# Kernel tuning notes

Hardware: AMD Instinct MI355X
Metric: run time of the kernel (lower is better)

The kernel has to match this reference:

```python
import jax, jax.numpy as jnp
import numpy as np

TAU = 1.0      # temperature for gumbel-softmax
EPS = 1e-12    # F.normalize eps


def _l2norm(v, axis):
    n = jnp.sqrt(jnp.sum(v * v, axis=axis, keepdims=True))
    return v / jnp.maximum(n, EPS)


def setup_inputs() -> dict:
    key = jax.random.key(0)
    k1, k2, k3, k4 = jax.random.split(key, 4)
    b, c, h, w, n = 8, 512, 64, 64, 1024
    x = jax.random.normal(k1, (b, c, h, w), dtype=jnp.float32)
    centers = jax.random.normal(k2, (n, c), dtype=jnp.float32)          # VQ codebook
    clusters = jax.random.normal(k3, (n, c), dtype=jnp.float32)         # ClusterLookup param
    gumbel_noise = jax.random.gumbel(k4, (b, n, h, w), dtype=jnp.float32)
    return {"x": x, "centers": centers, "clusters": clusters, "gumbel_noise": gumbel_noise}


def reference(x, centers, clusters, gumbel_noise):
    # similarity logits: [b, n, h, w]
    inner = jnp.einsum('bchw,nc->bnhw', x, centers)
    # hard gumbel-softmax (straight-through) over code dim
    y_soft = jax.nn.softmax((inner + gumbel_noise) / TAU, axis=1)
    idx = jnp.argmax(y_soft, axis=1)                                     # [b, h, w]
    y_hard = jax.nn.one_hot(idx, centers.shape[0], axis=1, dtype=y_soft.dtype)
    one_hot = y_hard - jax.lax.stop_gradient(y_soft) + y_soft            # [b, n, h, w]
    # quantized features: codebook lookup expressed as einsum
    z_q = jnp.einsum('bnhw,nd->bdhw', one_hot, centers)                  # [b, c, h, w]
    # ClusterLookup(z_q, alpha=None, is_direct=False)
    nf = _l2norm(z_q, axis=1)
    ncl = _l2norm(clusters, axis=1)
    ip = jnp.einsum('bchw,nc->bnhw', nf, ncl)                            # cluster logits
    preds = jnp.argmax(ip, axis=1)                                       # [b, h, w] int
    probs = jax.nn.one_hot(preds, clusters.shape[0], axis=1, dtype=ip.dtype)
    cluster_loss = -jnp.mean(jnp.sum(probs * ip, axis=1))
    return (cluster_loss, preds, ip, z_q)
```

## Files before the change

### kernel.cpp

```cpp
#include <hip/hip_runtime.h>
#include <math.h>

#define C 512
#define HW 4096
#define N 1024
#define NPIX 32768
#define MARGIN 2.0f

typedef short s16x8 __attribute__((ext_vector_type(8)));
typedef float f32x4 __attribute__((ext_vector_type(4)));

__device__ inline unsigned short f2bf(float f) {
    unsigned int u = __float_as_uint(f);
    return (unsigned short)((u + 0x7FFFu + ((u >> 16) & 1u)) >> 16);
}
__device__ inline float h2f(unsigned short u) {
    _Float16 h; __builtin_memcpy(&h, &u, 2); return (float)h;
}
__device__ inline unsigned short f2h(float f) {
    _Float16 h = (_Float16)f; unsigned short u; __builtin_memcpy(&u, &h, 2); return u;
}
__device__ inline unsigned int mono(float v) {
    unsigned int u = __float_as_uint(v);
    return (u & 0x80000000u) ? ~u : (u | 0x80000000u);
}
__device__ inline void gload_lds16(const void* gsrc, void* ldst) {
    __builtin_amdgcn_global_load_lds(
        (const __attribute__((address_space(1))) unsigned int*)gsrc,
        (__attribute__((address_space(3))) unsigned int*)ldst, 16, 0, 0);
}

__global__ __launch_bounds__(64) void k_norms(const float* __restrict__ centers,
                                              const float* __restrict__ clusters,
                                              float* __restrict__ cnorm,
                                              float* __restrict__ clnorm) {
    int r = blockIdx.x;
    const float* src = (r < N) ? (centers + (size_t)r * C) : (clusters + (size_t)(r - N) * C);
    int lane = threadIdx.x;
    float s = 0.f;
    for (int k = lane; k < C; k += 64) { float v = src[k]; s += v * v; }
    #pragma unroll
    for (int m = 1; m < 64; m <<= 1) s += __shfl_xor(s, m, 64);
    if (lane == 0) {
        float nrm = sqrtf(s);
        if (nrm < 1e-12f) nrm = 1e-12f;
        if (r < N) cnorm[r] = nrm; else clnorm[r - N] = nrm;
    }
}

__global__ __launch_bounds__(256) void k_gemmM(const float* __restrict__ centers,
                                               const float* __restrict__ clusters,
                                               const float* __restrict__ cnorm,
                                               const float* __restrict__ clnorm,
                                               float* __restrict__ M) {
    __shared__ float as[32][68];
    __shared__ float bs[32][68];
    int tid = threadIdx.x;
    int tx = tid & 15, ty = tid >> 4;
    int i0 = blockIdx.x * 64, j0 = blockIdx.y * 64;
    int lrow = tid >> 2, lkq = (tid & 3) * 8;
    float acc[4][4] = {};
    for (int kc = 0; kc < C; kc += 32) {
        float4 a0 = *(const float4*)(centers + (size_t)(i0 + lrow) * C + kc + lkq);
        float4 a1 = *(const float4*)(centers + (size_t)(i0 + lrow) * C + kc + lkq + 4);
        float4 b0 = *(const float4*)(clusters + (size_t)(j0 + lrow) * C + kc + lkq);
        float4 b1 = *(const float4*)(clusters + (size_t)(j0 + lrow) * C + kc + lkq + 4);
        __syncthreads();
        as[lkq+0][lrow]=a0.x; as[lkq+1][lrow]=a0.y; as[lkq+2][lrow]=a0.z; as[lkq+3][lrow]=a0.w;
        as[lkq+4][lrow]=a1.x; as[lkq+5][lrow]=a1.y; as[lkq+6][lrow]=a1.z; as[lkq+7][lrow]=a1.w;
        bs[lkq+0][lrow]=b0.x; bs[lkq+1][lrow]=b0.y; bs[lkq+2][lrow]=b0.z; bs[lkq+3][lrow]=b0.w;
        bs[lkq+4][lrow]=b1.x; bs[lkq+5][lrow]=b1.y; bs[lkq+6][lrow]=b1.z; bs[lkq+7][lrow]=b1.w;
        __syncthreads();
        #pragma unroll
        for (int k = 0; k < 32; k += 4) {
            float av[4][4], bv[4][4];
            #pragma unroll
            for (int kk = 0; kk < 4; ++kk) {
                float4 ta = *(const float4*)&as[k+kk][tx*4];
                float4 tb = *(const float4*)&bs[k+kk][ty*4];
                av[kk][0]=ta.x; av[kk][1]=ta.y; av[kk][2]=ta.z; av[kk][3]=ta.w;
                bv[kk][0]=tb.x; bv[kk][1]=tb.y; bv[kk][2]=tb.z; bv[kk][3]=tb.w;
            }
            #pragma unroll
            for (int kk = 0; kk < 4; ++kk)
                #pragma unroll
                for (int ii = 0; ii < 4; ++ii)
                    #pragma unroll
                    for (int jj = 0; jj < 4; ++jj)
                        acc[ii][jj] = fmaf(av[kk][ii], bv[kk][jj], acc[ii][jj]);
        }
    }
    float rci[4], rcj[4];
    #pragma unroll
    for (int ii = 0; ii < 4; ++ii) rci[ii] = cnorm[i0 + tx*4 + ii];
    #pragma unroll
    for (int jj = 0; jj < 4; ++jj) rcj[jj] = clnorm[j0 + ty*4 + jj];
    #pragma unroll
    for (int ii = 0; ii < 4; ++ii)
        #pragma unroll
        for (int jj = 0; jj < 4; ++jj)
            M[(size_t)(i0 + tx*4 + ii) * N + (j0 + ty*4 + jj)] = acc[ii][jj] / (rci[ii] * rcj[jj]);
}

__global__ __launch_bounds__(256) void k_rowstat(const float* __restrict__ M,
                                                 float* __restrict__ rowmax,
                                                 int* __restrict__ rowarg) {
    __shared__ float sv[256];
    __shared__ int   sa[256];
    int i = blockIdx.x, tid = threadIdx.x;
    float bv = -INFINITY; int ba = 0;
    for (int j = tid; j < N; j += 256) {
        float v = M[(size_t)i * N + j];
        if (v > bv || (v == bv && j < ba)) { bv = v; ba = j; }
    }
    sv[tid] = bv; sa[tid] = ba;
    __syncthreads();
    for (int s = 128; s > 0; s >>= 1) {
        if (tid < s) {
            float v = sv[tid + s]; int a = sa[tid + s];
            if (v > sv[tid] || (v == sv[tid] && a < sa[tid])) { sv[tid] = v; sa[tid] = a; }
        }
        __syncthreads();
    }
    if (tid == 0) { rowmax[i] = sv[0]; rowarg[i] = sa[0]; }
}

__global__ __launch_bounds__(256) void k_prepT(const float* __restrict__ x,
                                               float* __restrict__ xT) {
    __shared__ float t[64][65];
    int bidx = blockIdx.x;
    int pt = bidx & 63, kt = (bidx >> 6) & 7, b = bidx >> 9;
    int r = threadIdx.x >> 4, c4 = (threadIdx.x & 15) * 4;
    const float* src = x + ((size_t)b * C + kt * 64) * HW + pt * 64;
    #pragma unroll
    for (int rr = 0; rr < 4; ++rr) {
        int row = rr * 16 + r;
        float4 v = *(const float4*)(src + (size_t)row * HW + c4);
        t[row][c4] = v.x; t[row][c4+1] = v.y; t[row][c4+2] = v.z; t[row][c4+3] = v.w;
    }
    __syncthreads();
    float* dst = xT + ((size_t)b * HW + pt * 64) * C + kt * 64;
    #pragma unroll
    for (int rr = 0; rr < 4; ++rr) {
        int row = rr * 16 + r;
        float4 v = { t[c4][row], t[c4+1][row], t[c4+2][row], t[c4+3][row] };
        *(float4*)(dst + (size_t)row * C + c4) = v;
    }
}

__global__ __launch_bounds__(64) void k_cenfrag(const float* __restrict__ centers,
                                                unsigned short* __restrict__ cenB) {
    int f = blockIdx.x;
    int nt = f >> 4, kt = f & 15;
    int lane = threadIdx.x;
    int r = lane & 15, g = lane >> 4;
    const float* src = centers + (size_t)(nt * 16 + r) * C + kt * 32 + g * 4;
    float4 lo = *(const float4*)src;
    float4 hi = *(const float4*)(src + 16);
    union { unsigned short us[8]; uint4 q; } u;
    u.us[0]=f2bf(lo.x); u.us[1]=f2bf(lo.y); u.us[2]=f2bf(lo.z); u.us[3]=f2bf(lo.w);
    u.us[4]=f2bf(hi.x); u.us[5]=f2bf(hi.y); u.us[6]=f2bf(hi.z); u.us[7]=f2bf(hi.w);
    *(uint4*)(cenB + ((size_t)f * 64 + lane) * 8) = u.q;
}

__global__ __launch_bounds__(256, 3) void k_fused(const float* __restrict__ xT,
                                                  const unsigned short* __restrict__ cenB,
                                                  const float* __restrict__ gumbel,
                                                  const float* __restrict__ centers,
                                                  int* __restrict__ idxb) {
    __shared__ unsigned short cen[2][8192];
    __shared__ float glds[2][1024];
    __shared__ unsigned long long pixkey[64];
    __shared__ unsigned int candlist[4][256];
    __shared__ int candcount[4];

    int tid = threadIdx.x;
    int lane = tid & 63, w = tid >> 6;
    int r = lane & 15, g = lane >> 4;

    int p0 = blockIdx.x * 64;
    int b = p0 >> 12, hw0 = p0 & (HW - 1);

    if (tid < 64) pixkey[tid] = 0ull;
    if (tid < 4) candcount[tid] = 0;

    int grow_ = tid >> 4;
    int gcol_ = ((tid ^ (tid >> 4)) & 15) * 4;
    const float* gbase = gumbel + (size_t)b * N * HW + hw0 + gcol_;

    {
        const char* src = (const char*)cenB + w * 4096 + lane * 16;
        char* dst = (char*)&cen[0][0] + w * 4096;
        #pragma unroll
        for (int i = 0; i < 4; ++i) gload_lds16(src + i * 1024, dst + i * 1024);
        gload_lds16(gbase + (size_t)grow_ * HW, (char*)&glds[0][0] + tid * 16);
    }

    s16x8 a[16];
    {
        const float* xrow = xT + (size_t)(p0 + w * 16 + r) * C;
        #pragma unroll
        for (int kt = 0; kt < 16; ++kt) {
            float4 lo = *(const float4*)(xrow + kt * 32 + g * 4);
            float4 hi = *(const float4*)(xrow + kt * 32 + 16 + g * 4);
            s16x8 t;
            t[0]=(short)f2bf(lo.x); t[1]=(short)f2bf(lo.y); t[2]=(short)f2bf(lo.z); t[3]=(short)f2bf(lo.w);
            t[4]=(short)f2bf(hi.x); t[5]=(short)f2bf(hi.y); t[6]=(short)f2bf(hi.z); t[7]=(short)f2bf(hi.w);
            a[kt] = t;
        }
    }
    __syncthreads();

    float m4[4] = {-INFINITY, -INFINITY, -INFINITY, -INFINITY};
    int cur = 0;
    int gswz = r * 64 + ((((w << 2) + g) ^ r) << 2);

    for (int tc = 0; tc < 8; ++tc) {
        unsigned int keepH[16];
        #pragma unroll
        for (int s = 0; s < 8; ++s) {
            int t = tc * 8 + s;
            if (t < 63) {
                const char* src = (const char*)cenB + (size_t)(t + 1) * 16384 + w * 4096 + lane * 16;
                char* dst = (char*)&cen[cur ^ 1][0] + w * 4096;
                #pragma unroll
                for (int i = 0; i < 4; ++i) gload_lds16(src + i * 1024, dst + i * 1024);
                gload_lds16(gbase + (size_t)((t + 1) * 16 + grow_) * HW,
                            (char*)&glds[cur ^ 1][0] + tid * 16);
            }
            const s16x8* bp = (const s16x8*)&cen[cur][0] + lane;
            f32x4 acc0 = {0.f,0.f,0.f,0.f}, acc1 = {0.f,0.f,0.f,0.f};
            #pragma unroll
            for (int kt = 0; kt < 16; kt += 2) {
                acc0 = __builtin_amdgcn_mfma_f32_16x16x32_bf16(a[kt],   bp[kt*64],     acc0, 0,0,0);
                acc1 = __builtin_amdgcn_mfma_f32_16x16x32_bf16(a[kt+1], bp[(kt+1)*64], acc1, 0,0,0);
            }
            f32x4 gv = *(const f32x4*)&glds[cur][gswz];
            float v0 = acc0[0]+acc1[0]+gv[0], v1 = acc0[1]+acc1[1]+gv[1];
            float v2 = acc0[2]+acc1[2]+gv[2], v3 = acc0[3]+acc1[3]+gv[3];
            m4[0]=fmaxf(m4[0],v0); m4[1]=fmaxf(m4[1],v1);
            m4[2]=fmaxf(m4[2],v2); m4[3]=fmaxf(m4[3],v3);
            keepH[s*2]   = (unsigned int)f2h(v0) | ((unsigned int)f2h(v1) << 16);
            keepH[s*2+1] = (unsigned int)f2h(v2) | ((unsigned int)f2h(v3) << 16);
            __syncthreads();
            cur ^= 1;
        }
        #pragma unroll
        for (int s2 = 1; s2 < 16; s2 <<= 1) {
            #pragma unroll
            for (int j = 0; j < 4; ++j) m4[j] = fmaxf(m4[j], __shfl_xor(m4[j], s2, 64));
        }
        float thr[4];
        #pragma unroll
        for (int j = 0; j < 4; ++j) thr[j] = m4[j] - MARGIN;
        #pragma unroll
        for (int s = 0; s < 8; ++s) {
            int nn = ((tc * 8 + s) << 4) + r;
            #pragma unroll
            for (int j2 = 0; j2 < 2; ++j2) {
                unsigned int pk = keepH[s * 2 + j2];
                float lo = h2f((unsigned short)(pk & 0xFFFFu));
                float hi = h2f((unsigned short)(pk >> 16));
                if (lo >= thr[j2 * 2]) {
                    int pos = atomicAdd(&candcount[w], 1);
                    if (pos < 256) candlist[w][pos] =
                        (unsigned int)nn | ((unsigned int)(w * 16 + g * 4 + j2 * 2) << 10);
                }
                if (hi >= thr[j2 * 2 + 1]) {
                    int pos = atomicAdd(&candcount[w], 1);
                    if (pos < 256) candlist[w][pos] =
                        (unsigned int)nn | ((unsigned int)(w * 16 + g * 4 + j2 * 2 + 1) << 10);
                }
            }
        }
    }

    int cc = candcount[w]; if (cc > 256) cc = 256;
    int sl = lane & 15, cg = lane >> 4;
    for (int t0 = 0; t0 < cc; t0 += 4) {
        int c = t0 + cg;
        bool valid = c < cc;
        unsigned int e = candlist[w][valid ? c : 0];
        int n = (int)(e & 1023u), pl = (int)(e >> 10);
        const float* xr = xT + (size_t)(p0 + pl) * C;
        const float* cenr = centers + (size_t)n * C;
        float s = 0.f;
        #pragma unroll
        for (int m = 0; m < 8; ++m) {
            int G = sl + (m << 4);
            float4 xv = *(const float4*)(xr + (G << 2));
            float4 cv = *(const float4*)(cenr + (G << 2));
            s = fmaf(xv.x, cv.x, s); s = fmaf(xv.y, cv.y, s);
            s = fmaf(xv.z, cv.z, s); s = fmaf(xv.w, cv.w, s);
        }
        #pragma unroll
        for (int s2 = 1; s2 < 16; s2 <<= 1) s += __shfl_xor(s, s2, 64);
        if (valid && sl == 0) {
            float val = s + gumbel[((size_t)b * N + n) * HW + hw0 + pl];
            unsigned long long key = ((unsigned long long)mono(val) << 32) | (unsigned int)(1023 - n);
            atomicMax(&pixkey[pl], key);
        }
    }
    __syncthreads();
    if (tid < 64) idxb[p0 + tid] = 1023 - (int)(unsigned int)(pixkey[tid] & 0xFFFFFFFFull);
}

__global__ __launch_bounds__(256) void k_preds(const int* __restrict__ idxb,
                                               const float* __restrict__ rowmax,
                                               const int* __restrict__ rowarg,
                                               float* __restrict__ preds_out,
                                               float* __restrict__ partial) {
    __shared__ float sv[256];
    int gid = blockIdx.x * 256 + threadIdx.x;
    int i = idxb[gid];
    preds_out[gid] = (float)rowarg[i];
    sv[threadIdx.x] = rowmax[i];
    __syncthreads();
    for (int s = 128; s > 0; s >>= 1) {
        if (threadIdx.x < s) sv[threadIdx.x] += sv[threadIdx.x + s];
        __syncthreads();
    }
    if (threadIdx.x == 0) partial[blockIdx.x] = sv[0];
}

__global__ __launch_bounds__(256) void k_gather(const float* __restrict__ src, int ncols,
                                                const int* __restrict__ idx,
                                                float* __restrict__ dst) {
    __shared__ float rows[64][65];
    int tile = blockIdx.x;
    int col0 = blockIdx.y * 64;
    int tid = threadIdx.x;
    int lane = tid & 63, w = tid >> 6;
    int b = tile >> 6, hw0 = (tile & 63) << 6;
    #pragma unroll
    for (int r8 = 0; r8 < 16; ++r8) {
        int r = w * 16 + r8;
        int row = idx[tile * 64 + r];
        rows[r][lane] = src[(size_t)row * ncols + col0 + lane];
    }
    __syncthreads();
    #pragma unroll
    for (int jj = 0; jj < 16; ++jj) {
        int j = col0 + w * 16 + jj;
        dst[((size_t)b * ncols + j) * HW + hw0 + lane] = rows[lane][w * 16 + jj];
    }
}

__global__ __launch_bounds__(128) void k_loss(const float* __restrict__ partial,
                                              float* __restrict__ out) {
    __shared__ float sv[128];
    sv[threadIdx.x] = partial[threadIdx.x];
    __syncthreads();
    for (int s = 64; s > 0; s >>= 1) {
        if (threadIdx.x < s) sv[threadIdx.x] += sv[threadIdx.x + s];
        __syncthreads();
    }
    if (threadIdx.x == 0) out[0] = -(sv[0] / 32768.0f);
}

extern "C" void kernel_launch(void* const* d_in, const int* in_sizes, int n_in,
                              void* d_out, int out_size, void* d_ws, size_t ws_size,
                              hipStream_t stream) {
    const float* x        = (const float*)d_in[0];
    const float* centers  = (const float*)d_in[1];
    const float* clusters = (const float*)d_in[2];
    const float* gumbel   = (const float*)d_in[3];
    float* out = (float*)d_out;

    char* w = (char*)d_ws;
    int*   idxb    = (int*)w;
    float* cnorm   = (float*)(w + 131072);
    float* clnorm  = cnorm + 1024;
    float* rowmax  = clnorm + 1024;
    int*   rowarg  = (int*)(rowmax + 1024);
    float* partial = (float*)(rowarg + 1024);
    float* M       = (float*)(w + 262144);
    unsigned short* cenB = (unsigned short*)(w + 4456448);

    float* out_loss  = out;
    float* out_preds = out + 1;
    float* out_ip    = out + 1 + 32768;
    float* out_zq    = out + 1 + 32768 + (size_t)N * NPIX;

    float* xT = out_zq;

    k_norms  <<<2048, 64, 0, stream>>>(centers, clusters, cnorm, clnorm);
    k_gemmM  <<<dim3(16, 16), 256, 0, stream>>>(centers, clusters, cnorm, clnorm, M);
    k_rowstat<<<1024, 256, 0, stream>>>(M, rowmax, rowarg);
    k_cenfrag<<<1024, 64, 0, stream>>>(centers, cenB);
    k_prepT  <<<4096, 256, 0, stream>>>(x, xT);
    k_fused  <<<512, 256, 0, stream>>>(xT, cenB, gumbel, centers, idxb);
    k_preds  <<<128, 256, 0, stream>>>(idxb, rowmax, rowarg, out_preds, partial);
    k_gather <<<dim3(512, 16), 256, 0, stream>>>(M, N, idxb, out_ip);
    k_gather <<<dim3(512, 8),  256, 0, stream>>>(centers, C, idxb, out_zq);
    k_loss   <<<1, 128, 0, stream>>>(partial, out_loss);
}
```

Measured before the change: 298.4 us.

## Triple-buffer codebook and gumbel tiles with two-stage-ahead async prefetch

Replaces the double-buffered LDS pipeline for codebook fragments and gumbel noise with a three-buffer ring that prefetches two tiles ahead. It uses explicit vmcnt/lgkmcnt waits and raw s_barrier instead of __syncthreads, and issues the initial prefetch after the x-fragment loads. The goal is to hide global-to-LDS latency behind the MFMA work. In exchange, LDS use rises and launch bounds drop from 3 to 2 blocks per CU, which lowers occupancy. The hand-written waitcnt counts must match the number of outstanding loads exactly.

```diff
diff --git a/kernel.cpp b/kernel.cpp
--- a/kernel.cpp
+++ b/kernel.cpp
@@ -163,13 +163,13 @@
     *(uint4*)(cenB + ((size_t)f * 64 + lane) * 8) = u.q;
 }
 
-__global__ __launch_bounds__(256, 3) void k_fused(const float* __restrict__ xT,
+__global__ __launch_bounds__(256, 2) void k_fused(const float* __restrict__ xT,
                                                   const unsigned short* __restrict__ cenB,
                                                   const float* __restrict__ gumbel,
                                                   const float* __restrict__ centers,
                                                   int* __restrict__ idxb) {
-    __shared__ unsigned short cen[2][8192];
-    __shared__ float glds[2][1024];
+    __shared__ unsigned short cen[3][8192];
+    __shared__ float glds[3][1024];
     __shared__ unsigned long long pixkey[64];
     __shared__ unsigned int candlist[4][256];
     __shared__ int candcount[4];
@@ -183,18 +183,6 @@
 
     if (tid < 64) pixkey[tid] = 0ull;
     if (tid < 4) candcount[tid] = 0;
-
-    int grow_ = tid >> 4;
-    int gcol_ = ((tid ^ (tid >> 4)) & 15) * 4;
-    const float* gbase = gumbel + (size_t)b * N * HW + hw0 + gcol_;
-
-    {
-        const char* src = (const char*)cenB + w * 4096 + lane * 16;
-        char* dst = (char*)&cen[0][0] + w * 4096;
-        #pragma unroll
-        for (int i = 0; i < 4; ++i) gload_lds16(src + i * 1024, dst + i * 1024);
-        gload_lds16(gbase + (size_t)grow_ * HW, (char*)&glds[0][0] + tid * 16);
-    }
 
     s16x8 a[16];
     {
@@ -209,10 +197,30 @@
             a[kt] = t;
         }
     }
-    __syncthreads();
+
+    int grow_ = tid >> 4;
+    int gcol_ = ((tid ^ (tid >> 4)) & 15) * 4;
+    const float* gbase = gumbel + (size_t)b * N * HW + hw0 + gcol_;
+
+    #define STAGE(T, BUF) { \
+        const char* s_ = (const char*)cenB + (size_t)(T) * 16384 + w * 4096 + lane * 16; \
+        char* d_ = (char*)&cen[0][0] + (BUF) * 16384 + w * 4096; \
+        gload_lds16(s_, d_); gload_lds16(s_ + 1024, d_ + 1024); \
+        gload_lds16(s_ + 2048, d_ + 2048); gload_lds16(s_ + 3072, d_ + 3072); \
+        gload_lds16(gbase + (size_t)((T) * 16 + grow_) * HW, \
+                    (char*)&glds[0][0] + (BUF) * 4096 + tid * 16); \
+    }
+
+    __builtin_amdgcn_sched_barrier(0);
+    STAGE(0, 0);
+    STAGE(1, 1);
+    __builtin_amdgcn_sched_barrier(0);
+    asm volatile("s_waitcnt vmcnt(5)" ::: "memory");
+    __builtin_amdgcn_s_barrier();
+    __builtin_amdgcn_sched_barrier(0);
 
     float m4[4] = {-INFINITY, -INFINITY, -INFINITY, -INFINITY};
-    int cur = 0;
+    int c0 = 0;
     int gswz = r * 64 + ((((w << 2) + g) ^ r) << 2);
 
     for (int tc = 0; tc < 8; ++tc) {
@@ -220,30 +228,32 @@
         #pragma unroll
         for (int s = 0; s < 8; ++s) {
             int t = tc * 8 + s;
-            if (t < 63) {
-                const char* src = (const char*)cenB + (size_t)(t + 1) * 16384 + w * 4096 + lane * 16;
-                char* dst = (char*)&cen[cur ^ 1][0] + w * 4096;
-                #pragma unroll
-                for (int i = 0; i < 4; ++i) gload_lds16(src + i * 1024, dst + i * 1024);
-                gload_lds16(gbase + (size_t)((t + 1) * 16 + grow_) * HW,
-                            (char*)&glds[cur ^ 1][0] + tid * 16);
-            }
-            const s16x8* bp = (const s16x8*)&cen[cur][0] + lane;
+            const s16x8* bp = (const s16x8*)((char*)&cen[0][0] + c0 * 16384) + lane;
             f32x4 acc0 = {0.f,0.f,0.f,0.f}, acc1 = {0.f,0.f,0.f,0.f};
             #pragma unroll
             for (int kt = 0; kt < 16; kt += 2) {
                 acc0 = __builtin_amdgcn_mfma_f32_16x16x32_bf16(a[kt],   bp[kt*64],     acc0, 0,0,0);
                 acc1 = __builtin_amdgcn_mfma_f32_16x16x32_bf16(a[kt+1], bp[(kt+1)*64], acc1, 0,0,0);
             }
-            f32x4 gv = *(const f32x4*)&glds[cur][gswz];
+            f32x4 gv = *(const f32x4*)((const float*)&glds[0][0] + c0 * 1024 + gswz);
             float v0 = acc0[0]+acc1[0]+gv[0], v1 = acc0[1]+acc1[1]+gv[1];
             float v2 = acc0[2]+acc1[2]+gv[2], v3 = acc0[3]+acc1[3]+gv[3];
             m4[0]=fmaxf(m4[0],v0); m4[1]=fmaxf(m4[1],v1);
             m4[2]=fmaxf(m4[2],v2); m4[3]=fmaxf(m4[3],v3);
             keepH[s*2]   = (unsigned int)f2h(v0) | ((unsigned int)f2h(v1) << 16);
             keepH[s*2+1] = (unsigned int)f2h(v2) | ((unsigned int)f2h(v3) << 16);
-            __syncthreads();
-            cur ^= 1;
+            asm volatile("s_waitcnt lgkmcnt(0)" ::: "memory");
+            __builtin_amdgcn_sched_barrier(0);
+            __builtin_amdgcn_s_barrier();
+            __builtin_amdgcn_sched_barrier(0);
+            int c2 = c0 + 2; if (c2 >= 3) c2 -= 3;
+            if (t + 2 <= 63) { STAGE(t + 2, c2); }
+            __builtin_amdgcn_sched_barrier(0);
+            if (t + 2 <= 63)      { asm volatile("s_waitcnt vmcnt(5)" ::: "memory"); }
+            else if (t + 1 <= 63) { asm volatile("s_waitcnt vmcnt(0)" ::: "memory"); }
+            __builtin_amdgcn_s_barrier();
+            __builtin_amdgcn_sched_barrier(0);
+            c0 = c0 + 1; if (c0 >= 3) c0 -= 3;
         }
         #pragma unroll
         for (int s2 = 1; s2 < 16; s2 <<= 1) {
@@ -274,6 +284,7 @@
             }
         }
     }
+    #undef STAGE
 
     int cc = candcount[w]; if (cc > 256) cc = 256;
     int sl = lane & 15, cg = lane >> 4;
```

New measurement: 257.5 us. 13.7% less time.
